# Kernel tuning notes

Measured on AMD Instinct MI355X. Metric: run time of the kernel, lower is better.

The kernel has to match this reference:

```python
import jax, jax.numpy as jnp
import numpy as np
from jax import lax

C, NH, HC, HID, P = 192, 8, 64, 512, 16
B, H, W = 2, 128, 128
EPS = 1e-5


def setup_inputs() -> dict:
    key = jax.random.key(0)
    ks = jax.random.split(key, 12)
    f = lambda i, shape: jax.random.normal(ks[i], shape, jnp.float32) * 0.05
    return dict(
        x=jax.random.normal(ks[0], (B, C, H, W), jnp.float32),
        ln1_g=jnp.ones((C,), jnp.float32), ln1_b=jnp.zeros((C,), jnp.float32),
        wq=f(1, (HID, C)), wk=f(2, (HID, C)), wv=f(3, (HID, C)),
        wo=f(4, (C, HID)), bo=jnp.zeros((C,), jnp.float32),
        dw_w=f(5, (C, 1, 3, 3)), dw_b=jnp.zeros((C,), jnp.float32),
        mlp_w=f(6, (C, 2 * C)), mlp_b=jnp.zeros((C,), jnp.float32),
        ln2_g=jnp.ones((C,), jnp.float32), ln2_b=jnp.zeros((C,), jnp.float32),
        c1_w=f(7, (C, C)), c1_b=jnp.zeros((C,), jnp.float32),
        res_w=f(8, (C, 1, 3, 3)), res_b=jnp.zeros((C,), jnp.float32),
        c2_w=f(9, (C, C)), c2_b=jnp.zeros((C,), jnp.float32),
    )


def ln_ch(x, g, b):
    # LayerNorm over the channel dim of an NCHW tensor (biased variance, like torch)
    m = x.mean(1, keepdims=True)
    v = ((x - m) ** 2).mean(1, keepdims=True)
    return (x - m) / jnp.sqrt(v + EPS) * g[None, :, None, None] + b[None, :, None, None]


def inorm(x):
    # InstanceNorm2d, affine=False
    m = x.mean((2, 3), keepdims=True)
    v = ((x - m) ** 2).mean((2, 3), keepdims=True)
    return (x - m) / jnp.sqrt(v + EPS)


def conv1x1(x, w, b=None):
    y = jnp.einsum('oc,bchw->bohw', w, x)
    return y if b is None else y + b[None, :, None, None]


def dwconv(x, w, b):
    y = lax.conv_general_dilated(x, w, (1, 1), 'SAME',
                                 feature_group_count=x.shape[1],
                                 dimension_numbers=('NCHW', 'OIHW', 'NCHW'))
    return y + b[None, :, None, None]


def res_block(x, w, b):
    return jax.nn.gelu(inorm(dwconv(x, w, b)), approximate=False) + x


def dpsa(x, ln_g, ln_b, wq, wk, wv, wo, bo):
    Bs, _, Hs, Ws = x.shape
    xn = ln_ch(x, ln_g, ln_b)

    def proj(w):  # -> (B*NH, H, W, HC)
        t = jnp.einsum('oc,bchw->bohw', w, xn)
        return t.reshape(Bs * NH, HC, Hs, Ws).transpose(0, 2, 3, 1)

    l2n = lambda t: t / jnp.maximum(jnp.linalg.norm(t, axis=-1, keepdims=True), 1e-12)
    q = l2n(proj(wq))
    k = l2n(proj(wk))
    v = proj(wv)

    qs = q.sum((1, 2))                                   # (BH, HC)
    h_scores = jnp.einsum('bc,bhc->bh', qs, k.sum(2))    # (BH, H)
    w_scores = jnp.einsum('bc,bwc->bw', qs, k.sum(1))    # (BH, W)
    _, h_idx = lax.top_k(h_scores, P)
    _, w_idx = lax.top_k(w_scores, P)

    k = jnp.take_along_axis(k, h_idx[:, :, None, None], axis=1)   # (BH, P, W, HC)
    v = jnp.take_along_axis(v, h_idx[:, :, None, None], axis=1)
    k = jnp.take_along_axis(k, w_idx[:, None, :, None], axis=2)   # (BH, P, P, HC)
    v = jnp.take_along_axis(v, w_idx[:, None, :, None], axis=2)

    qf = q.reshape(Bs * NH, Hs * Ws, HC)
    kf = k.reshape(Bs * NH, P * P, HC)
    vf = v.reshape(Bs * NH, P * P, HC)
    attn = jax.nn.softmax(jnp.einsum('bqc,bkc->bqk', qf, kf), axis=-1)
    out = jnp.einsum('bqk,bkc->bqc', attn, vf)
    out = out.reshape(Bs, NH, Hs, Ws, HC).transpose(0, 1, 4, 2, 3).reshape(Bs, NH * HC, Hs, Ws)
    return conv1x1(out, wo, bo)


def reference(x, ln1_g, ln1_b, wq, wk, wv, wo, bo, dw_w, dw_b, mlp_w, mlp_b,
              ln2_g, ln2_b, c1_w, c1_b, res_w, res_b, c2_w, c2_b):
    global_branch = dpsa(x, ln1_g, ln1_b, wq, wk, wv, wo, bo)
    local_branch = dwconv(x, dw_w, dw_b)
    f = jnp.concatenate((local_branch, global_branch), axis=1)
    f = conv1x1(f, mlp_w, mlp_b) + x
    y = ln_ch(f, ln2_g, ln2_b)
    y = jax.nn.gelu(inorm(conv1x1(y, c1_w, c1_b)), approximate=False)
    y = res_block(y, res_w, res_b)
    y = inorm(conv1x1(y, c2_w, c2_b))
    return y
```

## Files before the change

kernel.cpp:

```cpp
#include <hip/hip_runtime.h>
#include <math.h>

constexpr int kC   = 192;
constexpr int kNH  = 8;
constexpr int kHC  = 64;
constexpr int kHID = 512;
constexpr int kP   = 16;
constexpr int kB   = 2;
constexpr int kH   = 128;
constexpr int kW   = 128;
constexpr int kHW  = kH * kW;
constexpr int kN   = kB * kHW;
constexpr float kEPS = 1e-5f;

typedef __attribute__((ext_vector_type(8))) short bf16x8;
typedef __attribute__((ext_vector_type(4))) float f32x4;

__device__ inline unsigned short f2bf(float f) {
    unsigned int u = __builtin_bit_cast(unsigned int, f);
    unsigned int r = (u + 0x7FFFu + ((u >> 16) & 1u)) >> 16;
    return (unsigned short)r;
}
__device__ inline float bf2f(unsigned short u) {
    return __builtin_bit_cast(float, (unsigned int)u << 16);
}
__device__ inline unsigned int cvtpk(float lo, float hi) {
    unsigned int r;
    asm("v_cvt_pk_bf16_f32 %0, %1, %2" : "=v"(r) : "v"(lo), "v"(hi));
    return r;
}
__device__ inline unsigned long long pk4(float a, float b, float c, float d) {
    return (unsigned long long)cvtpk(a, b) | ((unsigned long long)cvtpk(c, d) << 32);
}
__device__ inline f32x4 ubf4(unsigned long long u) {
    f32x4 r;
    r[0] = bf2f((unsigned short)u);
    r[1] = bf2f((unsigned short)(u >> 16));
    r[2] = bf2f((unsigned short)(u >> 32));
    r[3] = bf2f((unsigned short)(u >> 48));
    return r;
}

__global__ void prep_kernel(float* __restrict__ acc,
                            const float* wq, const float* wk, const float* wm,
                            const float* c1, const float* c2,
                            unsigned short* wqb, unsigned short* wkb,
                            unsigned short* mlpb1, unsigned short* c1b, unsigned short* c2b)
{
    int i = blockIdx.x * 256 + threadIdx.x;
    if (i < 2304) { acc[i] = 0.f; return; }
    i -= 2304;
    if (i < 98304) { wqb[i] = f2bf(wq[i]); return; }
    i -= 98304;
    if (i < 98304) { wkb[i] = f2bf(wk[i]); return; }
    i -= 98304;
    if (i < 36864) { int o = i / 192, k = i - o * 192; mlpb1[i] = f2bf(wm[o * 384 + k]); return; }
    i -= 36864;
    if (i < 36864) { c1b[i] = f2bf(c1[i]); return; }
    i -= 36864;
    if (i < 36864) { c2b[i] = f2bf(c2[i]); return; }
}

__global__ void wfuse_kernel(const float* __restrict__ mlp_w, const float* __restrict__ wo,
                             const float* __restrict__ mlp_b, const float* __restrict__ bo,
                             unsigned short* __restrict__ w2pb, float* __restrict__ bp2)
{
    int i = blockIdx.x * 256 + threadIdx.x;
    int o = i >> 9, j = i & 511;
    const float* a = mlp_w + o * 384 + 192;
    float s = 0.f;
    for (int c = 0; c < 192; ++c) s += a[c] * wo[c * 512 + j];
    w2pb[o * 512 + j] = f2bf(s);
    if (j == 0) {
        float t = mlp_b[o];
        for (int c = 0; c < 192; ++c) t += a[c] * bo[c];
        bp2[o] = t;
    }
}

__global__ __launch_bounds__(256) void txln_kernel(const float* __restrict__ x,
                                                   float* __restrict__ xp,
                                                   unsigned short* __restrict__ xnb,
                                                   const float* __restrict__ g,
                                                   const float* __restrict__ bb)
{
    __shared__ float tile[192][65];
    __shared__ float red[2][4][64];
    __shared__ float pms[64], prs[64];
    int hw0 = blockIdx.x * 64;
    int b   = blockIdx.y;
    int tid = threadIdx.x;
    for (int i = tid; i < 192 * 64; i += 256) {
        int c = i >> 6, p = i & 63;
        tile[c][p] = x[(size_t)(b * kC + c) * kHW + hw0 + p];
    }
    __syncthreads();
    {
        int p = tid & 63, qt = tid >> 6;
        float s = 0.f, ss = 0.f;
        for (int c = qt * 48; c < qt * 48 + 48; ++c) {
            float v = tile[c][p]; s += v; ss += v * v;
        }
        red[0][qt][p] = s; red[1][qt][p] = ss;
    }
    __syncthreads();
    if (tid < 64) {
        float s  = red[0][0][tid] + red[0][1][tid] + red[0][2][tid] + red[0][3][tid];
        float ss = red[1][0][tid] + red[1][1][tid] + red[1][2][tid] + red[1][3][tid];
        float m = s * (1.0f / kC);
        float var = ss * (1.0f / kC) - m * m;
        pms[tid] = m;
        prs[tid] = rsqrtf(var + kEPS);
    }
    __syncthreads();
    for (int i = tid; i < 64 * 192; i += 256) {
        int p = i / 192, c = i - p * 192;
        float raw = tile[c][p];
        size_t oi = (size_t)(b * kHW + hw0 + p) * kC + c;
        xp[oi] = raw;
        xnb[oi] = f2bf((raw - pms[p]) * prs[p] * g[c] + bb[c]);
    }
}

__global__ void ln_pm_bf16_kernel(const unsigned short* __restrict__ in,
                                  unsigned short* __restrict__ out,
                                  const float* __restrict__ g, const float* __restrict__ bb)
{
    int n = blockIdx.x * 256 + threadIdx.x;
    if (n >= kN) return;
    const unsigned long long* ip = (const unsigned long long*)(in + (size_t)n * kC);
    float s = 0.f, ss = 0.f;
#pragma unroll
    for (int r = 0; r < 48; ++r) {
        f32x4 v = ubf4(ip[r]);
        s  += (v[0] + v[1]) + (v[2] + v[3]);
        ss += (v[0]*v[0] + v[1]*v[1]) + (v[2]*v[2] + v[3]*v[3]);
    }
    float m  = s * (1.0f / kC);
    float var = ss * (1.0f / kC) - m * m;
    float rs = rsqrtf(var + kEPS);
    unsigned long long* op = (unsigned long long*)(out + (size_t)n * kC);
#pragma unroll
    for (int r = 0; r < 48; ++r) {
        f32x4 v = ubf4(ip[r]);
        f32x4 gg = *(const f32x4*)(g + r * 4);
        f32x4 bv = *(const f32x4*)(bb + r * 4);
        op[r] = pk4((v[0]-m)*rs*gg[0] + bv[0], (v[1]-m)*rs*gg[1] + bv[1],
                    (v[2]-m)*rs*gg[2] + bv[2], (v[3]-m)*rs*gg[3] + bv[3]);
    }
}

#define MGEMM_CORE(KVAL, APTR, BPTR)                                              \
    {                                                                             \
        const unsigned short* Ap = APTR;                                          \
        const unsigned short* Bp = BPTR;                                          \
        _Pragma("unroll 2")                                                       \
        for (int k = 0; k < KVAL; k += 32) {                                      \
            bf16x8 a0 = *(const bf16x8*)(Ap + k);                                 \
            bf16x8 a1 = *(const bf16x8*)(Ap + (size_t)16 * KVAL + k);             \
            bf16x8 b0 = *(const bf16x8*)(Bp + k);                                 \
            bf16x8 b1 = *(const bf16x8*)(Bp + (size_t)16 * KVAL + k);             \
            bf16x8 b2 = *(const bf16x8*)(Bp + (size_t)32 * KVAL + k);             \
            bf16x8 b3 = *(const bf16x8*)(Bp + (size_t)48 * KVAL + k);             \
            acc[0][0] = __builtin_amdgcn_mfma_f32_16x16x32_bf16(a0, b0, acc[0][0], 0, 0, 0); \
            acc[0][1] = __builtin_amdgcn_mfma_f32_16x16x32_bf16(a0, b1, acc[0][1], 0, 0, 0); \
            acc[0][2] = __builtin_amdgcn_mfma_f32_16x16x32_bf16(a0, b2, acc[0][2], 0, 0, 0); \
            acc[0][3] = __builtin_amdgcn_mfma_f32_16x16x32_bf16(a0, b3, acc[0][3], 0, 0, 0); \
            acc[1][0] = __builtin_amdgcn_mfma_f32_16x16x32_bf16(a1, b0, acc[1][0], 0, 0, 0); \
            acc[1][1] = __builtin_amdgcn_mfma_f32_16x16x32_bf16(a1, b1, acc[1][1], 0, 0, 0); \
            acc[1][2] = __builtin_amdgcn_mfma_f32_16x16x32_bf16(a1, b2, acc[1][2], 0, 0, 0); \
            acc[1][3] = __builtin_amdgcn_mfma_f32_16x16x32_bf16(a1, b3, acc[1][3], 0, 0, 0); \
        }                                                                         \
    }

__global__ __launch_bounds__(256) void mgemm_is_kernel(
    const unsigned short* __restrict__ A, const unsigned short* __restrict__ B,
    unsigned short* __restrict__ out, const float* __restrict__ bias,
    float* __restrict__ accp)
{
    __shared__ float sa[2][64], qa[2][64];
    int nB = blockIdx.x * 128, oB = blockIdx.y * 64;
    int w = threadIdx.x >> 6, lane = threadIdx.x & 63;
    int l15 = lane & 15, g = lane >> 4;
    int wm = w & 1, wn = w >> 1;

    f32x4 acc[2][4];
#pragma unroll
    for (int mt = 0; mt < 2; ++mt)
#pragma unroll
        for (int nt = 0; nt < 4; ++nt) acc[mt][nt] = (f32x4){0.f,0.f,0.f,0.f};

    MGEMM_CORE(192, A + (size_t)(oB + wm * 32 + l15) * 192 + 8 * g,
                    B + (size_t)(nB + wn * 64 + l15) * 192 + 8 * g);

    f32x4 vv[2][4];
#pragma unroll
    for (int mt = 0; mt < 2; ++mt)
#pragma unroll
        for (int nt = 0; nt < 4; ++nt) {
            int o = oB + wm * 32 + mt * 16 + 4 * g;
            int n = nB + wn * 64 + nt * 16 + l15;
            f32x4 v = acc[mt][nt] + *(const f32x4*)(bias + o);
            vv[mt][nt] = v;
            *(unsigned long long*)(out + (size_t)n * kC + o) = pk4(v[0], v[1], v[2], v[3]);
        }
    float s2[2][4] = {}, q2[2][4] = {};
#pragma unroll
    for (int mt = 0; mt < 2; ++mt)
#pragma unroll
        for (int nt = 0; nt < 4; ++nt)
#pragma unroll
            for (int r = 0; r < 4; ++r) {
                float v = vv[mt][nt][r];
                s2[mt][r] += v; q2[mt][r] += v * v;
            }
#pragma unroll
    for (int off = 1; off < 16; off <<= 1)
#pragma unroll
        for (int mt = 0; mt < 2; ++mt)
#pragma unroll
            for (int r = 0; r < 4; ++r) {
                s2[mt][r] += __shfl_xor(s2[mt][r], off);
                q2[mt][r] += __shfl_xor(q2[mt][r], off);
            }
    if (l15 == 0)
#pragma unroll
        for (int mt = 0; mt < 2; ++mt)
#pragma unroll
            for (int r = 0; r < 4; ++r) {
                int ol = wm * 32 + mt * 16 + 4 * g + r;
                sa[wn][ol] = s2[mt][r];
                qa[wn][ol] = q2[mt][r];
            }
    __syncthreads();
    if (threadIdx.x < 128) {
        int ol = threadIdx.x & 63, st = threadIdx.x >> 6;
        float v = st ? (qa[0][ol] + qa[1][ol]) : (sa[0][ol] + sa[1][ol]);
        int b = nB >> 14;
        atomicAdd(&accp[(size_t)(b * kC + oB + ol) * 2 + st], v);
    }
}

__global__ __launch_bounds__(256) void mgemm_mlp_kernel(
    const unsigned short* __restrict__ A1, const unsigned short* __restrict__ B1,
    const unsigned short* __restrict__ A2, const unsigned short* __restrict__ B2,
    unsigned short* __restrict__ out, const float* __restrict__ bp2,
    const float* __restrict__ res)
{
    int nB = blockIdx.x * 128, oB = blockIdx.y * 64;
    int w = threadIdx.x >> 6, lane = threadIdx.x & 63;
    int l15 = lane & 15, g = lane >> 4;
    int wm = w & 1, wn = w >> 1;

    f32x4 acc[2][4];
#pragma unroll
    for (int mt = 0; mt < 2; ++mt)
#pragma unroll
        for (int nt = 0; nt < 4; ++nt) acc[mt][nt] = (f32x4){0.f,0.f,0.f,0.f};

    MGEMM_CORE(192, A1 + (size_t)(oB + wm * 32 + l15) * 192 + 8 * g,
                    B1 + (size_t)(nB + wn * 64 + l15) * 192 + 8 * g);
    MGEMM_CORE(512, A2 + (size_t)(oB + wm * 32 + l15) * 512 + 8 * g,
                    B2 + (size_t)(nB + wn * 64 + l15) * 512 + 8 * g);

#pragma unroll
    for (int mt = 0; mt < 2; ++mt)
#pragma unroll
        for (int nt = 0; nt < 4; ++nt) {
            int o = oB + wm * 32 + mt * 16 + 4 * g;
            int n = nB + wn * 64 + nt * 16 + l15;
            f32x4 v = acc[mt][nt];
            v[0] += bp2[o]; v[1] += bp2[o+1]; v[2] += bp2[o+2]; v[3] += bp2[o+3];
            v += *(const f32x4*)(res + (size_t)n * kC + o);
            *(unsigned long long*)(out + (size_t)n * kC + o) = pk4(v[0], v[1], v[2], v[3]);
        }
}

__global__ __launch_bounds__(256) void mgemm_l2_kernel(
    const unsigned short* __restrict__ A, const unsigned short* __restrict__ B,
    unsigned short* __restrict__ out, float* __restrict__ red_out)
{
    __shared__ float ssq[2][2][4][16];
    __shared__ float rbuf[2][2][4][2][4];
    int nB = blockIdx.x * 128, oB = blockIdx.y * 64;
    int w = threadIdx.x >> 6, lane = threadIdx.x & 63;
    int l15 = lane & 15, g = lane >> 4;
    int wm = w & 1, wn = w >> 1;

    f32x4 acc[2][4];
#pragma unroll
    for (int mt = 0; mt < 2; ++mt)
#pragma unroll
        for (int nt = 0; nt < 4; ++nt) acc[mt][nt] = (f32x4){0.f,0.f,0.f,0.f};

    MGEMM_CORE(192, A + (size_t)(oB + wm * 32 + l15) * 192 + 8 * g,
                    B + (size_t)(nB + wn * 64 + l15) * 192 + 8 * g);

#pragma unroll
    for (int nt = 0; nt < 4; ++nt) {
        float s = 0.f;
#pragma unroll
        for (int mt = 0; mt < 2; ++mt) {
            f32x4 a = acc[mt][nt];
            s += (a[0]*a[0] + a[1]*a[1]) + (a[2]*a[2] + a[3]*a[3]);
        }
        s += __shfl_xor(s, 16);
        s += __shfl_xor(s, 32);
        if (g == 0) ssq[wm][wn][nt][l15] = s;
    }
    __syncthreads();

    float sc[4];
#pragma unroll
    for (int nt = 0; nt < 4; ++nt) {
        float ss2 = ssq[0][wn][nt][l15] + ssq[1][wn][nt][l15];
        sc[nt] = 1.0f / fmaxf(sqrtf(ss2), 1e-12f);
    }

#pragma unroll
    for (int nt = 0; nt < 4; ++nt) {
        int n = nB + wn * 64 + nt * 16 + l15;
#pragma unroll
        for (int mt = 0; mt < 2; ++mt) {
            int o = oB + wm * 32 + mt * 16 + 4 * g;
            f32x4 v = acc[mt][nt];
            *(unsigned long long*)(out + (size_t)n * kHID + o) =
                pk4(v[0]*sc[nt], v[1]*sc[nt], v[2]*sc[nt], v[3]*sc[nt]);
        }
    }

    float sred[2][4] = {};
#pragma unroll
    for (int nt = 0; nt < 4; ++nt)
#pragma unroll
        for (int mt = 0; mt < 2; ++mt) {
            f32x4 a = acc[mt][nt];
            sred[mt][0] += a[0] * sc[nt];
            sred[mt][1] += a[1] * sc[nt];
            sred[mt][2] += a[2] * sc[nt];
            sred[mt][3] += a[3] * sc[nt];
        }
#pragma unroll
    for (int off = 1; off < 16; off <<= 1)
#pragma unroll
        for (int mt = 0; mt < 2; ++mt)
#pragma unroll
            for (int r = 0; r < 4; ++r)
                sred[mt][r] += __shfl_xor(sred[mt][r], off);
    if (l15 == 0)
#pragma unroll
        for (int mt = 0; mt < 2; ++mt)
#pragma unroll
            for (int r = 0; r < 4; ++r)
                rbuf[wm][wn][g][mt][r] = sred[mt][r];
    __syncthreads();
    if (threadIdx.x < 64) {
        int o = threadIdx.x;
        int wm2 = o >> 5, mt2 = (o >> 4) & 1, g2 = (o >> 2) & 3, r2 = o & 3;
        float v = rbuf[wm2][0][g2][mt2][r2] + rbuf[wm2][1][g2][mt2][r2];
        int row = (nB & (kHW - 1)) >> 7;
        int b = nB >> 14;
        int bh = b * 8 + blockIdx.y;
        red_out[((size_t)(bh * 128 + row)) * 64 + o] = v;
    }
}

__global__ void sum_h_kernel(const unsigned short* __restrict__ buf, float* __restrict__ out)
{
    int w = blockIdx.x, bh = blockIdx.y, hc = threadIdx.x;
    int b = bh >> 3, nh = bh & 7;
    const unsigned short* p = buf + (size_t)(b * kHW + w) * kHID + nh * kHC + hc;
    float s = 0.f;
    for (int h = 0; h < kH; ++h) s += bf2f(p[(size_t)h * kW * kHID]);
    out[((size_t)bh * kW + w) * kHC + hc] = s;
}

__global__ void score_topk_kernel(const float* __restrict__ qpart,
                                  const float* __restrict__ ksum_h,
                                  const float* __restrict__ ksum_w,
                                  int* __restrict__ hidx, int* __restrict__ widx)
{
    __shared__ float qsl[2][64];
    __shared__ float hs[128], ws[128];
    int bh = blockIdx.x;
    int tid = threadIdx.x;
    int hc = tid & 63, grp = tid >> 6;
    {
        const float* qp = qpart + ((size_t)bh * 128 + grp * 64) * 64 + hc;
        float s = 0.f;
        for (int i = 0; i < 64; ++i) s += qp[(size_t)i * 64];
        qsl[grp][hc] = s;
    }
    __syncthreads();
    if (tid < 64) qsl[0][tid] += qsl[1][tid];
    __syncthreads();
    {
        const float* kh = ksum_h + ((size_t)bh * 128 + tid) * 64;
        const float* kw = ksum_w + ((size_t)bh * 128 + tid) * 64;
        float sh = 0.f, sw = 0.f;
        for (int c = 0; c < 64; ++c) {
            float q = qsl[0][c];
            sh += q * kh[c];
            sw += q * kw[c];
        }
        hs[tid] = sh; ws[tid] = sw;
    }
    __syncthreads();
    int sel = tid >> 6;
    const float* sc = sel ? ws : hs;
    int* out = (sel ? widx : hidx) + bh * kP;
    int lane = tid & 63;
    float v0 = sc[lane], v1 = sc[lane + 64];
    int i0 = lane, i1 = lane + 64;
    for (int p = 0; p < kP; ++p) {
        float bv; int bi;
        if (v1 > v0) { bv = v1; bi = i1; } else { bv = v0; bi = i0; }
#pragma unroll
        for (int off = 1; off < 64; off <<= 1) {
            float ov = __shfl_xor(bv, off);
            int   oi = __shfl_xor(bi, off);
            if (ov > bv || (ov == bv && oi < bi)) { bv = ov; bi = oi; }
        }
        if (lane == 0) out[p] = bi;
        if (i0 == bi) v0 = -INFINITY;
        if (i1 == bi) v1 = -INFINITY;
    }
}

__global__ void gather_kv_kernel(const unsigned short* __restrict__ kpb,
                                 const unsigned short* __restrict__ xnb,
                                 const float* __restrict__ wv,
                                 const int* __restrict__ hidx, const int* __restrict__ widx,
                                 unsigned short* __restrict__ kf, unsigned short* __restrict__ vfT)
{
    int bh = blockIdx.y, p1 = blockIdx.x;
    int b = bh >> 3, nh = bh & 7;
    int hc = threadIdx.x & 63, pg = threadIdx.x >> 6;
    int hrow = hidx[bh * kP + p1];
    int o = nh * kHC + hc;
    const float* wvp = wv + (size_t)o * kC;
    for (int p2 = pg; p2 < kP; p2 += 4) {
        int wcol = widx[bh * kP + p2];
        int n = b * kHW + hrow * kW + wcol;
        int kidx = p1 * kP + p2;
        kf[((size_t)bh * 256 + kidx) * 64 + hc] = kpb[(size_t)n * kHID + nh * kHC + hc];
        const unsigned int* xr = (const unsigned int*)(xnb + (size_t)n * kC);
        float s = 0.f;
        for (int c2 = 0; c2 < kC / 2; ++c2) {
            unsigned int u = xr[c2];
            s += wvp[c2 * 2]     * bf2f((unsigned short)(u & 0xffff));
            s += wvp[c2 * 2 + 1] * bf2f((unsigned short)(u >> 16));
        }
        vfT[((size_t)bh * 64 + hc) * 256 + kidx] = f2bf(s);
    }
}

__global__ __launch_bounds__(256) void attn_kernel(
    const unsigned short* __restrict__ qpb, unsigned short* __restrict__ ob,
    const unsigned short* __restrict__ kf, const unsigned short* __restrict__ vfT)
{
    __shared__ unsigned short pls[64 * 272];
    __shared__ float lred[4][4][16];

    int bh = blockIdx.y; int b = bh >> 3, nh = bh & 7;
    int n0 = b * kHW + blockIdx.x * 64;
    int tid = threadIdx.x;
    int w = tid >> 6, lane = tid & 63, l15 = lane & 15, g = lane >> 4;

    bf16x8 bq[4][2];
#pragma unroll
    for (int nt = 0; nt < 4; ++nt)
#pragma unroll
        for (int kt = 0; kt < 2; ++kt)
            bq[nt][kt] = *(const bf16x8*)(qpb + (size_t)(n0 + nt * 16 + l15) * kHID
                                          + nh * kHC + kt * 32 + 8 * g);

    const unsigned short* kfb = kf + (size_t)bh * 256 * 64;
    bf16x8 ak[4][2];
#pragma unroll
    for (int mt = 0; mt < 4; ++mt)
#pragma unroll
        for (int kt = 0; kt < 2; ++kt)
            ak[mt][kt] = *(const bf16x8*)&kfb[(size_t)(w * 64 + mt * 16 + l15) * 64 + kt * 32 + 8 * g];

    f32x4 acc[4][4];
#pragma unroll
    for (int mt = 0; mt < 4; ++mt)
#pragma unroll
        for (int nt = 0; nt < 4; ++nt) acc[mt][nt] = (f32x4){0.f,0.f,0.f,0.f};

#pragma unroll
    for (int kt = 0; kt < 2; ++kt)
#pragma unroll
        for (int mt = 0; mt < 4; ++mt)
#pragma unroll
            for (int nt = 0; nt < 4; ++nt)
                acc[mt][nt] = __builtin_amdgcn_mfma_f32_16x16x32_bf16(
                    ak[mt][kt], bq[nt][kt], acc[mt][nt], 0, 0, 0);

    float lpart[4] = {0.f, 0.f, 0.f, 0.f};
#pragma unroll
    for (int mt = 0; mt < 4; ++mt)
#pragma unroll
        for (int nt = 0; nt < 4; ++nt) {
            float e0 = __expf(acc[mt][nt][0]);
            float e1 = __expf(acc[mt][nt][1]);
            float e2 = __expf(acc[mt][nt][2]);
            float e3 = __expf(acc[mt][nt][3]);
            lpart[nt] += (e0 + e1) + (e2 + e3);
            int qq = nt * 16 + l15;
            int k0 = w * 64 + mt * 16 + 4 * g;
            *(unsigned long long*)&pls[qq * 272 + k0] = pk4(e0, e1, e2, e3);
        }
#pragma unroll
    for (int nt = 0; nt < 4; ++nt) {
        lpart[nt] += __shfl_xor(lpart[nt], 16);
        lpart[nt] += __shfl_xor(lpart[nt], 32);
    }
    if (g == 0)
#pragma unroll
        for (int nt = 0; nt < 4; ++nt) lred[w][nt][l15] = lpart[nt];
    __syncthreads();

    const unsigned short* vfb = vfT + (size_t)bh * 64 * 256;
    f32x4 oacc[4];
#pragma unroll
    for (int nt = 0; nt < 4; ++nt) oacc[nt] = (f32x4){0.f,0.f,0.f,0.f};

#pragma unroll
    for (int ks = 0; ks < 8; ++ks) {
        bf16x8 av = *(const bf16x8*)&vfb[(size_t)(w * 16 + l15) * 256 + ks * 32 + 8 * g];
#pragma unroll
        for (int nt = 0; nt < 4; ++nt) {
            bf16x8 bp = *(const bf16x8*)&pls[(nt * 16 + l15) * 272 + ks * 32 + 8 * g];
            oacc[nt] = __builtin_amdgcn_mfma_f32_16x16x32_bf16(av, bp, oacc[nt], 0, 0, 0);
        }
    }

#pragma unroll
    for (int nt = 0; nt < 4; ++nt) {
        float l = lred[0][nt][l15] + lred[1][nt][l15] + lred[2][nt][l15] + lred[3][nt][l15];
        float inv = 1.0f / l;
        int qq = nt * 16 + l15;
        int hc0 = w * 16 + 4 * g;
        *(unsigned long long*)(ob + (size_t)(n0 + qq) * kHID + nh * kHC + hc0) =
            pk4(oacc[nt][0] * inv, oacc[nt][1] * inv, oacc[nt][2] * inv, oacc[nt][3] * inv);
    }
}

template<int INBF16>
__global__ void dwconv_pm_kernel(const void* __restrict__ in, unsigned short* __restrict__ out,
                                 const float* __restrict__ wt, const float* __restrict__ bias)
{
    int idx = blockIdx.x * 256 + threadIdx.x;
    int n = idx / 48;
    int c0 = (idx - n * 48) * 4;
    int hw = n & (kHW - 1);
    int h = hw >> 7, ww = hw & 127;
    f32x4 s = *(const f32x4*)(bias + c0);
#pragma unroll
    for (int dy = -1; dy <= 1; ++dy) {
        int hh = h + dy;
        if (hh < 0 || hh >= kH) continue;
#pragma unroll
        for (int dx = -1; dx <= 1; ++dx) {
            int wx = ww + dx;
            if (wx < 0 || wx >= kW) continue;
            f32x4 v;
            if (INBF16)
                v = ubf4(*(const unsigned long long*)((const unsigned short*)in
                          + (size_t)(n + dy * kW + dx) * kC + c0));
            else
                v = *(const f32x4*)((const float*)in + (size_t)(n + dy * kW + dx) * kC + c0);
            int t = (dy + 1) * 3 + (dx + 1);
            s[0] += v[0] * wt[(c0 + 0) * 9 + t];
            s[1] += v[1] * wt[(c0 + 1) * 9 + t];
            s[2] += v[2] * wt[(c0 + 2) * 9 + t];
            s[3] += v[3] * wt[(c0 + 3) * 9 + t];
        }
    }
    *(unsigned long long*)(out + (size_t)n * kC + c0) = pk4(s[0], s[1], s[2], s[3]);
}

__global__ void istats_bf16_kernel(const unsigned short* __restrict__ in, float* __restrict__ acc)
{
    int n0 = blockIdx.x * 64;
    int b = n0 >> 14;
    int c = threadIdx.x;
    float s = 0.f, ss = 0.f;
    for (int p = 0; p < 64; ++p) {
        float v = bf2f(in[(size_t)(n0 + p) * kC + c]);
        s += v; ss += v * v;
    }
    atomicAdd(&acc[(size_t)(b * kC + c) * 2],     s);
    atomicAdd(&acc[(size_t)(b * kC + c) * 2 + 1], ss);
}

__device__ inline void inorm_ms(const float* acc, int b, int c, float& m, float& rs)
{
    float s  = acc[(size_t)(b * kC + c) * 2];
    float ss = acc[(size_t)(b * kC + c) * 2 + 1];
    m = s * (1.0f / kHW);
    float var = ss * (1.0f / kHW) - m * m;
    rs = rsqrtf(var + kEPS);
}

template<int MODE>
__global__ void apply_pm_kernel(const unsigned short* __restrict__ in, const float* __restrict__ acc,
                                unsigned short* __restrict__ out, const unsigned short* __restrict__ addsrc)
{
    int idx = blockIdx.x * 256 + threadIdx.x;
    int n = idx / 48;
    int c0 = (idx - n * 48) * 4;
    int b = n >> 14;
    f32x4 v = ubf4(*(const unsigned long long*)(in + (size_t)n * kC + c0));
    f32x4 r;
#pragma unroll
    for (int j = 0; j < 4; ++j) {
        float m, rs;
        inorm_ms(acc, b, c0 + j, m, rs);
        float x = (v[j] - m) * rs;
        r[j] = 0.5f * x * (1.0f + erff(x * 0.70710678118654752f));
    }
    if (MODE == 1)
        r += ubf4(*(const unsigned long long*)(addsrc + (size_t)n * kC + c0));
    *(unsigned long long*)(out + (size_t)n * kC + c0) = pk4(r[0], r[1], r[2], r[3]);
}

__global__ __launch_bounds__(256) void final_kernel(const unsigned short* __restrict__ in,
                                                    const float* __restrict__ acc,
                                                    float* __restrict__ out)
{
    __shared__ unsigned short tile[192][68];
    int n0 = blockIdx.x * 64;
    int b = n0 >> 14;
    int hw0 = n0 & (kHW - 1);
    int tid = threadIdx.x;
    for (int i = tid; i < 64 * 48; i += 256) {
        int p = i / 48, cq = i - p * 48;
        unsigned long long u = *(const unsigned long long*)(in + (size_t)(n0 + p) * kC + cq * 4);
        tile[cq * 4 + 0][p] = (unsigned short)u;
        tile[cq * 4 + 1][p] = (unsigned short)(u >> 16);
        tile[cq * 4 + 2][p] = (unsigned short)(u >> 32);
        tile[cq * 4 + 3][p] = (unsigned short)(u >> 48);
    }
    __syncthreads();
    for (int i = tid; i < 192 * 16; i += 256) {
        int c = i >> 4, grp = i & 15;
        float m, rs;
        inorm_ms(acc, b, c, m, rs);
        f32x4 o;
#pragma unroll
        for (int j = 0; j < 4; ++j)
            o[j] = (bf2f(tile[c][grp * 4 + j]) - m) * rs;
        *(f32x4*)(out + (size_t)(b * kC + c) * kHW + hw0 + grp * 4) = o;
    }
}

extern "C" void kernel_launch(void* const* d_in, const int* in_sizes, int n_in,
                              void* d_out, int out_size, void* d_ws, size_t ws_size,
                              hipStream_t stream)
{
    const float* x     = (const float*)d_in[0];
    const float* ln1_g = (const float*)d_in[1];
    const float* ln1_b = (const float*)d_in[2];
    const float* wq    = (const float*)d_in[3];
    const float* wk    = (const float*)d_in[4];
    const float* wv    = (const float*)d_in[5];
    const float* wo    = (const float*)d_in[6];
    const float* bo    = (const float*)d_in[7];
    const float* dw_w  = (const float*)d_in[8];
    const float* dw_b  = (const float*)d_in[9];
    const float* mlp_w = (const float*)d_in[10];
    const float* mlp_b = (const float*)d_in[11];
    const float* ln2_g = (const float*)d_in[12];
    const float* ln2_b = (const float*)d_in[13];
    const float* c1_w  = (const float*)d_in[14];
    const float* c1_b  = (const float*)d_in[15];
    const float* res_w = (const float*)d_in[16];
    const float* res_b = (const float*)d_in[17];
    const float* c2_w  = (const float*)d_in[18];
    const float* c2_b  = (const float*)d_in[19];

    char* base = (char*)d_ws;
    float* XP = (float*)(base);
    unsigned short* XNb = (unsigned short*)(base + 25165824);
    unsigned short* QPb = (unsigned short*)(base + 37748736);
    unsigned short* F   = QPb;
    unsigned short* T2  = QPb;
    unsigned short* KPb = (unsigned short*)(base + 71303168);
    unsigned short* OB  = KPb;
    unsigned short* Y2  = KPb;
    unsigned short* LB  = (unsigned short*)(base + 104857600);
    unsigned short* Y3  = LB;
    unsigned short* T1  = (unsigned short*)(base + 117440512);
    unsigned short* R   = T1;
    char* sm = base + 130023424;
    float* qpart  = (float*)(sm);                 sm += 524288;
    float* ksum_h = (float*)(sm);                 sm += 524288;
    float* ksum_w = (float*)(sm);                 sm += 524288;
    float* acc0   = (float*)(sm);                 sm += 3072;
    float* acc1   = (float*)(sm);                 sm += 3072;
    float* acc2   = (float*)(sm);                 sm += 3072;
    unsigned short* kf   = (unsigned short*)(sm); sm += 524288;
    unsigned short* vfT  = (unsigned short*)(sm); sm += 524288;
    unsigned short* wqb  = (unsigned short*)(sm); sm += 196608;
    unsigned short* wkb  = (unsigned short*)(sm); sm += 196608;
    unsigned short* mlpb1= (unsigned short*)(sm); sm += 73728;
    unsigned short* c1b  = (unsigned short*)(sm); sm += 73728;
    unsigned short* c2b  = (unsigned short*)(sm); sm += 73728;
    unsigned short* w2pb = (unsigned short*)(sm); sm += 196608;
    float* bp2 = (float*)(sm);                    sm += 1024;
    int* hidx = (int*)(sm);                       sm += 1024;
    int* widx = (int*)(sm);

    prep_kernel<<<1209, 256, 0, stream>>>(acc0, wq, wk, mlp_w, c1_w, c2_w,
                                          wqb, wkb, mlpb1, c1b, c2b);
    wfuse_kernel<<<384, 256, 0, stream>>>(mlp_w, wo, mlp_b, bo, w2pb, bp2);
    txln_kernel<<<dim3(kHW / 64, kB), 256, 0, stream>>>(x, XP, XNb, ln1_g, ln1_b);

    mgemm_l2_kernel<<<dim3(kN / 128, kNH), 256, 0, stream>>>(wqb, XNb, QPb, qpart);
    mgemm_l2_kernel<<<dim3(kN / 128, kNH), 256, 0, stream>>>(wkb, XNb, KPb, ksum_h);
    sum_h_kernel<<<dim3(kW, 16), 64, 0, stream>>>(KPb, ksum_w);
    score_topk_kernel<<<16, 128, 0, stream>>>(qpart, ksum_h, ksum_w, hidx, widx);
    gather_kv_kernel<<<dim3(kP, 16), 256, 0, stream>>>(KPb, XNb, wv, hidx, widx, kf, vfT);
    attn_kernel<<<dim3(kHW / 64, 16), 256, 0, stream>>>(QPb, OB, kf, vfT);

    dwconv_pm_kernel<0><<<(kN * 48) / 256, 256, 0, stream>>>(XP, LB, dw_w, dw_b);
    mgemm_mlp_kernel<<<dim3(kN / 128, kC / 64), 256, 0, stream>>>(mlpb1, LB, w2pb, OB, F, bp2, XP);

    ln_pm_bf16_kernel<<<kN / 256, 256, 0, stream>>>(F, XNb, ln2_g, ln2_b);
    mgemm_is_kernel<<<dim3(kN / 128, kC / 64), 256, 0, stream>>>(c1b, XNb, T1, c1_b, acc0);
    apply_pm_kernel<0><<<(kN * 48) / 256, 256, 0, stream>>>(T1, acc0, Y2, nullptr);
    dwconv_pm_kernel<1><<<(kN * 48) / 256, 256, 0, stream>>>(Y2, R, res_w, res_b);
    istats_bf16_kernel<<<kN / 64, 192, 0, stream>>>(R, acc1);
    apply_pm_kernel<1><<<(kN * 48) / 256, 256, 0, stream>>>(R, acc1, Y3, Y2);
    mgemm_is_kernel<<<dim3(kN / 128, kC / 64), 256, 0, stream>>>(c2b, Y3, T2, c2_b, acc2);
    final_kernel<<<kN / 64, 256, 0, stream>>>(T2, acc2, (float*)d_out);
}
```

Measured before the change: 497.2 us.

## Store raw input as bf16, split LN rows, parallelize sum_h, swizzle attention LDS

The raw input copy is now stored as bf16 rather than fp32. This halves the traffic for the dwconv and the mlp residual read, at some cost in residual precision. LayerNorm2 now uses four threads per pixel with shuffle reductions and keeps the values in registers instead of reloading them. sum_h splits the H reduction across four warps. The attention kernel's LDS tile drops its padding in favour of an XOR swizzle to avoid bank conflicts.

```diff
diff --git a/kernel.cpp b/kernel.cpp
--- a/kernel.cpp
+++ b/kernel.cpp
@@ -79,7 +79,7 @@
 }
 
 __global__ __launch_bounds__(256) void txln_kernel(const float* __restrict__ x,
-                                                   float* __restrict__ xp,
+                                                   unsigned short* __restrict__ xpb,
                                                    unsigned short* __restrict__ xnb,
                                                    const float* __restrict__ g,
                                                    const float* __restrict__ bb)
@@ -117,7 +117,7 @@
         int p = i / 192, c = i - p * 192;
         float raw = tile[c][p];
         size_t oi = (size_t)(b * kHW + hw0 + p) * kC + c;
-        xp[oi] = raw;
+        xpb[oi] = f2bf(raw);
         xnb[oi] = f2bf((raw - pms[p]) * prs[p] * g[c] + bb[c]);
     }
 }
@@ -126,27 +126,29 @@
                                   unsigned short* __restrict__ out,
                                   const float* __restrict__ g, const float* __restrict__ bb)
 {
-    int n = blockIdx.x * 256 + threadIdx.x;
-    if (n >= kN) return;
-    const unsigned long long* ip = (const unsigned long long*)(in + (size_t)n * kC);
+    int t = blockIdx.x * 256 + threadIdx.x;
+    int n = t >> 2, q = t & 3;
+    const unsigned long long* ip = (const unsigned long long*)(in + (size_t)n * kC) + q * 12;
+    f32x4 v[12];
     float s = 0.f, ss = 0.f;
 #pragma unroll
-    for (int r = 0; r < 48; ++r) {
-        f32x4 v = ubf4(ip[r]);
-        s  += (v[0] + v[1]) + (v[2] + v[3]);
-        ss += (v[0]*v[0] + v[1]*v[1]) + (v[2]*v[2] + v[3]*v[3]);
-    }
+    for (int r = 0; r < 12; ++r) {
+        v[r] = ubf4(ip[r]);
+        s  += (v[r][0] + v[r][1]) + (v[r][2] + v[r][3]);
+        ss += (v[r][0]*v[r][0] + v[r][1]*v[r][1]) + (v[r][2]*v[r][2] + v[r][3]*v[r][3]);
+    }
+    s  += __shfl_xor(s, 1);  s  += __shfl_xor(s, 2);
+    ss += __shfl_xor(ss, 1); ss += __shfl_xor(ss, 2);
     float m  = s * (1.0f / kC);
     float var = ss * (1.0f / kC) - m * m;
     float rs = rsqrtf(var + kEPS);
-    unsigned long long* op = (unsigned long long*)(out + (size_t)n * kC);
-#pragma unroll
-    for (int r = 0; r < 48; ++r) {
-        f32x4 v = ubf4(ip[r]);
-        f32x4 gg = *(const f32x4*)(g + r * 4);
-        f32x4 bv = *(const f32x4*)(bb + r * 4);
-        op[r] = pk4((v[0]-m)*rs*gg[0] + bv[0], (v[1]-m)*rs*gg[1] + bv[1],
-                    (v[2]-m)*rs*gg[2] + bv[2], (v[3]-m)*rs*gg[3] + bv[3]);
+    unsigned long long* op = (unsigned long long*)(out + (size_t)n * kC) + q * 12;
+#pragma unroll
+    for (int r = 0; r < 12; ++r) {
+        f32x4 gg = *(const f32x4*)(g + q * 48 + r * 4);
+        f32x4 bv = *(const f32x4*)(bb + q * 48 + r * 4);
+        op[r] = pk4((v[r][0]-m)*rs*gg[0] + bv[0], (v[r][1]-m)*rs*gg[1] + bv[1],
+                    (v[r][2]-m)*rs*gg[2] + bv[2], (v[r][3]-m)*rs*gg[3] + bv[3]);
     }
 }
 
@@ -245,7 +247,7 @@
     const unsigned short* __restrict__ A1, const unsigned short* __restrict__ B1,
     const unsigned short* __restrict__ A2, const unsigned short* __restrict__ B2,
     unsigned short* __restrict__ out, const float* __restrict__ bp2,
-    const float* __restrict__ res)
+    const unsigned short* __restrict__ res)
 {
     int nB = blockIdx.x * 128, oB = blockIdx.y * 64;
     int w = threadIdx.x >> 6, lane = threadIdx.x & 63;
@@ -271,7 +273,7 @@
             int n = nB + wn * 64 + nt * 16 + l15;
             f32x4 v = acc[mt][nt];
             v[0] += bp2[o]; v[1] += bp2[o+1]; v[2] += bp2[o+2]; v[3] += bp2[o+3];
-            v += *(const f32x4*)(res + (size_t)n * kC + o);
+            v += ubf4(*(const unsigned long long*)(res + (size_t)n * kC + o));
             *(unsigned long long*)(out + (size_t)n * kC + o) = pk4(v[0], v[1], v[2], v[3]);
         }
 }
@@ -367,12 +369,18 @@
 
 __global__ void sum_h_kernel(const unsigned short* __restrict__ buf, float* __restrict__ out)
 {
-    int w = blockIdx.x, bh = blockIdx.y, hc = threadIdx.x;
+    __shared__ float red[4][64];
+    int w = blockIdx.x, bh = blockIdx.y;
+    int hc = threadIdx.x & 63, seg = threadIdx.x >> 6;
     int b = bh >> 3, nh = bh & 7;
-    const unsigned short* p = buf + (size_t)(b * kHW + w) * kHID + nh * kHC + hc;
+    const unsigned short* p = buf + (size_t)(b * kHW + seg * 32 * kW + w) * kHID + nh * kHC + hc;
     float s = 0.f;
-    for (int h = 0; h < kH; ++h) s += bf2f(p[(size_t)h * kW * kHID]);
-    out[((size_t)bh * kW + w) * kHC + hc] = s;
+    for (int h = 0; h < 32; ++h) s += bf2f(p[(size_t)h * kW * kHID]);
+    red[seg][hc] = s;
+    __syncthreads();
+    if (threadIdx.x < 64)
+        out[((size_t)bh * kW + w) * kHC + threadIdx.x] =
+            red[0][threadIdx.x] + red[1][threadIdx.x] + red[2][threadIdx.x] + red[3][threadIdx.x];
 }
 
 __global__ void score_topk_kernel(const float* __restrict__ qpart,
@@ -459,7 +467,7 @@
     const unsigned short* __restrict__ qpb, unsigned short* __restrict__ ob,
     const unsigned short* __restrict__ kf, const unsigned short* __restrict__ vfT)
 {
-    __shared__ unsigned short pls[64 * 272];
+    __shared__ unsigned short pls[64 * 256];
     __shared__ float lred[4][4][16];
 
     int bh = blockIdx.y; int b = bh >> 3, nh = bh & 7;
@@ -510,7 +518,8 @@
             lpart[nt] += (e0 + e1) + (e2 + e3);
             int qq = nt * 16 + l15;
             int k0 = w * 64 + mt * 16 + 4 * g;
-            *(unsigned long long*)&pls[qq * 272 + k0] = pk4(e0, e1, e2, e3);
+            int kx = k0 ^ ((qq & 7) << 3);
+            *(unsigned long long*)&pls[qq * 256 + kx] = pk4(e0, e1, e2, e3);
         }
 #pragma unroll
     for (int nt = 0; nt < 4; ++nt) {
@@ -532,7 +541,9 @@
         bf16x8 av = *(const bf16x8*)&vfb[(size_t)(w * 16 + l15) * 256 + ks * 32 + 8 * g];
 #pragma unroll
         for (int nt = 0; nt < 4; ++nt) {
-            bf16x8 bp = *(const bf16x8*)&pls[(nt * 16 + l15) * 272 + ks * 32 + 8 * g];
+            int qq = nt * 16 + l15;
+            int kx = (ks * 32 + 8 * g) ^ ((qq & 7) << 3);
+            bf16x8 bp = *(const bf16x8*)&pls[qq * 256 + kx];
             oacc[nt] = __builtin_amdgcn_mfma_f32_16x16x32_bf16(av, bp, oacc[nt], 0, 0, 0);
         }
     }
@@ -548,8 +559,8 @@
     }
 }
 
-template<int INBF16>
-__global__ void dwconv_pm_kernel(const void* __restrict__ in, unsigned short* __restrict__ out,
+__global__ void dwconv_pm_kernel(const unsigned short* __restrict__ in,
+                                 unsigned short* __restrict__ out,
                                  const float* __restrict__ wt, const float* __restrict__ bias)
 {
     int idx = blockIdx.x * 256 + threadIdx.x;
@@ -566,12 +577,7 @@
         for (int dx = -1; dx <= 1; ++dx) {
             int wx = ww + dx;
             if (wx < 0 || wx >= kW) continue;
-            f32x4 v;
-            if (INBF16)
-                v = ubf4(*(const unsigned long long*)((const unsigned short*)in
-                          + (size_t)(n + dy * kW + dx) * kC + c0));
-            else
-                v = *(const f32x4*)((const float*)in + (size_t)(n + dy * kW + dx) * kC + c0);
+            f32x4 v = ubf4(*(const unsigned long long*)(in + (size_t)(n + dy * kW + dx) * kC + c0));
             int t = (dy + 1) * 3 + (dx + 1);
             s[0] += v[0] * wt[(c0 + 0) * 9 + t];
             s[1] += v[1] * wt[(c0 + 1) * 9 + t];
@@ -683,7 +689,7 @@
     const float* c2_b  = (const float*)d_in[19];
 
     char* base = (char*)d_ws;
-    float* XP = (float*)(base);
+    unsigned short* XPb = (unsigned short*)(base);
     unsigned short* XNb = (unsigned short*)(base + 25165824);
     unsigned short* QPb = (unsigned short*)(base + 37748736);
     unsigned short* F   = QPb;
@@ -717,22 +723,22 @@
     prep_kernel<<<1209, 256, 0, stream>>>(acc0, wq, wk, mlp_w, c1_w, c2_w,
                                           wqb, wkb, mlpb1, c1b, c2b);
     wfuse_kernel<<<384, 256, 0, stream>>>(mlp_w, wo, mlp_b, bo, w2pb, bp2);
-    txln_kernel<<<dim3(kHW / 64, kB), 256, 0, stream>>>(x, XP, XNb, ln1_g, ln1_b);
+    txln_kernel<<<dim3(kHW / 64, kB), 256, 0, stream>>>(x, XPb, XNb, ln1_g, ln1_b);
 
     mgemm_l2_kernel<<<dim3(kN / 128, kNH), 256, 0, stream>>>(wqb, XNb, QPb, qpart);
     mgemm_l2_kernel<<<dim3(kN / 128, kNH), 256, 0, stream>>>(wkb, XNb, KPb, ksum_h);
-    sum_h_kernel<<<dim3(kW, 16), 64, 0, stream>>>(KPb, ksum_w);
+    sum_h_kernel<<<dim3(kW, 16), 256, 0, stream>>>(KPb, ksum_w);
     score_topk_kernel<<<16, 128, 0, stream>>>(qpart, ksum_h, ksum_w, hidx, widx);
     gather_kv_kernel<<<dim3(kP, 16), 256, 0, stream>>>(KPb, XNb, wv, hidx, widx, kf, vfT);
     attn_kernel<<<dim3(kHW / 64, 16), 256, 0, stream>>>(QPb, OB, kf, vfT);
 
-    dwconv_pm_kernel<0><<<(kN * 48) / 256, 256, 0, stream>>>(XP, LB, dw_w, dw_b);
-    mgemm_mlp_kernel<<<dim3(kN / 128, kC / 64), 256, 0, stream>>>(mlpb1, LB, w2pb, OB, F, bp2, XP);
-
-    ln_pm_bf16_kernel<<<kN / 256, 256, 0, stream>>>(F, XNb, ln2_g, ln2_b);
+    dwconv_pm_kernel<<<(kN * 48) / 256, 256, 0, stream>>>(XPb, LB, dw_w, dw_b);
+    mgemm_mlp_kernel<<<dim3(kN / 128, kC / 64), 256, 0, stream>>>(mlpb1, LB, w2pb, OB, F, bp2, XPb);
+
+    ln_pm_bf16_kernel<<<(kN * 4) / 256, 256, 0, stream>>>(F, XNb, ln2_g, ln2_b);
     mgemm_is_kernel<<<dim3(kN / 128, kC / 64), 256, 0, stream>>>(c1b, XNb, T1, c1_b, acc0);
     apply_pm_kernel<0><<<(kN * 48) / 256, 256, 0, stream>>>(T1, acc0, Y2, nullptr);
-    dwconv_pm_kernel<1><<<(kN * 48) / 256, 256, 0, stream>>>(Y2, R, res_w, res_b);
+    dwconv_pm_kernel<<<(kN * 48) / 256, 256, 0, stream>>>(Y2, R, res_w, res_b);
     istats_bf16_kernel<<<kN / 64, 192, 0, stream>>>(R, acc1);
     apply_pm_kernel<1><<<(kN * 48) / 256, 256, 0, stream>>>(R, acc1, Y3, Y2);
     mgemm_is_kernel<<<dim3(kN / 128, kC / 64), 256, 0, stream>>>(c2b, Y3, T2, c2_b, acc2);
```

After: 490.0 us. No clear change (-1.5%).
